# Kernel optimization log

Hardware: AMD Instinct MI355X
Metric: run time of the kernel (lower is better)

Reference implementation:

```python
import jax, jax.numpy as jnp
import numpy as np

B, S, D = 2, 2048, 768
HD = 64          # hardcoded head_dim in module
NH = D // HD     # 12 query heads
NKV = max(1, NH // 3)  # 4 kv heads
GROUPS = NH // NKV     # 3
WINDOW = 384
THETA = 10000.0
EPS = 1e-6


def setup_inputs() -> dict:
    key = jax.random.key(0)
    ks = jax.random.split(key, 5)
    return {
        "hidden_states": jax.random.normal(ks[0], (B, S, D), dtype=jnp.float32),
        "q_w": jax.random.normal(ks[1], (NH * HD, D), dtype=jnp.float32) * 0.02,
        "k_w": jax.random.normal(ks[2], (NKV * HD, D), dtype=jnp.float32) * 0.02,
        "v_w": jax.random.normal(ks[3], (NKV * HD, D), dtype=jnp.float32) * 0.02,
        "o_w": jax.random.normal(ks[4], (D, NH * HD), dtype=jnp.float32) * 0.02,
        "q_ln_w": jnp.ones((HD,), dtype=jnp.float32),
        "k_ln_w": jnp.ones((HD,), dtype=jnp.float32),
    }


def _rmsnorm(x, w):
    var = jnp.mean(jnp.square(x.astype(jnp.float32)), axis=-1, keepdims=True)
    return w * (x * jax.lax.rsqrt(var + EPS)).astype(x.dtype)


def _rotate_half(x):
    x1, x2 = jnp.split(x, 2, axis=-1)
    return jnp.concatenate((-x2, x1), axis=-1)


def _rope_cos_sin(seq_len, dtype):
    inv_freq = 1.0 / (THETA ** (jnp.arange(0, HD, 2, dtype=jnp.float32) / HD))
    t = jnp.arange(seq_len, dtype=jnp.float32)
    freqs = jnp.outer(t, inv_freq)            # [S, HD/2]
    emb = jnp.concatenate((freqs, freqs), -1)  # [S, HD]
    return jnp.cos(emb).astype(dtype), jnp.sin(emb).astype(dtype)


def reference(hidden_states, q_w, k_w, v_w, o_w, q_ln_w, k_ln_w):
    b, s, _ = hidden_states.shape
    # projections (nn.Linear: y = x @ W.T)
    q = hidden_states @ q_w.T   # [B,S,NH*HD]
    k = hidden_states @ k_w.T   # [B,S,NKV*HD]
    v = hidden_states @ v_w.T

    q = _rmsnorm(q.reshape(b, s, NH, HD), q_ln_w).transpose(0, 2, 1, 3)      # [B,NH,S,HD]
    k = _rmsnorm(k.reshape(b, s, NKV, HD), k_ln_w).transpose(0, 2, 1, 3)     # [B,NKV,S,HD]
    v = v.reshape(b, s, NKV, HD).transpose(0, 2, 1, 3)                       # [B,NKV,S,HD]

    cos, sin = _rope_cos_sin(s, q.dtype)  # [S,HD]
    cos = cos[None, None]
    sin = sin[None, None]
    q = q * cos + _rotate_half(q) * sin
    k = k * cos + _rotate_half(k) * sin

    # grouped-query repeat: [B,NKV,S,HD] -> [B,NH,S,HD]
    k = jnp.repeat(k, GROUPS, axis=1)
    v = jnp.repeat(v, GROUPS, axis=1)

    scores = jnp.einsum("bhqd,bhkd->bhqk", q, k) / np.sqrt(HD)
    # causal + sliding-window mask: allow i-WINDOW < j <= i
    idx = jnp.arange(s)
    rel = idx[None, :] - idx[:, None]  # j - i
    allowed = (rel <= 0) & (rel > -WINDOW)
    scores = jnp.where(allowed[None, None], scores, -jnp.inf)

    attn = jax.nn.softmax(scores.astype(jnp.float32), axis=-1).astype(q.dtype)
    out = jnp.einsum("bhqk,bhkd->bhqd", attn, v)       # [B,NH,S,HD]
    out = out.transpose(0, 2, 1, 3).reshape(b, s, NH * HD)
    return out @ o_w.T
```

## Files before the change

kernel.cpp:

```cpp
#include <hip/hip_runtime.h>
#include <hip/hip_bf16.h>

typedef __hip_bfloat16 bf16;
typedef __attribute__((ext_vector_type(8))) short bf16x8;
typedef __attribute__((ext_vector_type(4))) float f32x4;

#define MFMA16(a, b, c) __builtin_amdgcn_mfma_f32_16x16x32_bf16((a), (b), (c), 0, 0, 0)


__device__ __forceinline__ void st4bf(bf16* p, float4 v) {
    bf16 t[4];
    t[0] = __float2bfloat16(v.x); t[1] = __float2bfloat16(v.y);
    t[2] = __float2bfloat16(v.z); t[3] = __float2bfloat16(v.w);
    *reinterpret_cast<uint2*>(p) = *reinterpret_cast<const uint2*>(t);
}

__global__ __launch_bounds__(256) void k_prep(
    const float* __restrict__ hs, const float* __restrict__ qw,
    const float* __restrict__ kw, const float* __restrict__ vw,
    const float* __restrict__ ow,
    bf16* __restrict__ hsb, bf16* __restrict__ qwb, bf16* __restrict__ kwb,
    bf16* __restrict__ vwb, bf16* __restrict__ owb, float2* __restrict__ tab)
{
    const int bid = blockIdx.x, tid = threadIdx.x;
    const float* src; bf16* dst; int rel;
    if (bid < 3072)      { src = hs; dst = hsb; rel = bid; }
    else if (bid < 3648) { src = qw; dst = qwb; rel = bid - 3072; }
    else if (bid < 3840) { src = kw; dst = kwb; rel = bid - 3648; }
    else if (bid < 4032) { src = vw; dst = vwb; rel = bid - 3840; }
    else if (bid < 4608) { src = ow; dst = owb; rel = bid - 4032; }
    else {
        int i = (bid - 4608) * 256 + tid;
        int f = i & 31;
        float ang = (float)(i >> 5) * expf(-(float)f * 0.28782313662425572f);
        float sn, cs; sincosf(ang, &sn, &cs);
        tab[i] = make_float2(cs, sn);
        return;
    }
    int i = (rel * 256 + tid) * 4;
    float4 v = *reinterpret_cast<const float4*>(src + i);
    st4bf(dst + i, v);
}

__global__ __launch_bounds__(256) void k_qkv(
    const bf16* __restrict__ hsb, const bf16* __restrict__ qwb,
    const bf16* __restrict__ kwb, const bf16* __restrict__ vwb,
    const float* __restrict__ qln, const float* __restrict__ kln,
    const float2* __restrict__ tab,
    bf16* __restrict__ qo, bf16* __restrict__ ko, bf16* __restrict__ vto)
{
    __shared__ bf16 As[2][128 * 72];
    __shared__ bf16 Bs[2][128 * 72];
    const int tid = threadIdx.x;
    const int w = tid >> 6, l = tid & 63;
    const int lm = l & 15, lg = l >> 4;
    const int wr = w >> 1, wc = w & 1;
    const int m0 = blockIdx.x * 128;
    const int nblk = blockIdx.y;

    const bf16* wsrc; int kind, head;
    if (nblk < 6)      { wsrc = qwb + (size_t)nblk * 128 * 768;       kind = 0; head = nblk * 2 + wc; }
    else if (nblk < 8) { wsrc = kwb + (size_t)(nblk - 6) * 128 * 768; kind = 1; head = (nblk - 6) * 2 + wc; }
    else               { wsrc = vwb + (size_t)(nblk - 8) * 128 * 768; kind = 2; head = (nblk - 8) * 2 + wc; }

    const int sr = tid >> 1, scb = (tid & 1) * 8;
    const bf16* aptr = hsb  + (size_t)(m0 + sr) * 768 + scb;
    const bf16* bptr = wsrc + (size_t)sr * 768 + scb;

    bf16x8 ra[4], rb[4];
    #pragma unroll
    for (int j = 0; j < 4; ++j) {
        ra[j] = *(const bf16x8*)(aptr + j * 16);
        rb[j] = *(const bf16x8*)(bptr + j * 16);
    }
    #pragma unroll
    for (int j = 0; j < 4; ++j) {
        *(bf16x8*)(&As[0][sr * 72 + scb + j * 16]) = ra[j];
        *(bf16x8*)(&Bs[0][sr * 72 + scb + j * 16]) = rb[j];
    }
    __syncthreads();

    f32x4 acc[4][4] = {};
    for (int t = 0; t < 12; ++t) {
        const int p = t & 1;
        if (t < 11) {
            const int off = (t + 1) * 64;
            #pragma unroll
            for (int j = 0; j < 4; ++j) {
                ra[j] = *(const bf16x8*)(aptr + off + j * 16);
                rb[j] = *(const bf16x8*)(bptr + off + j * 16);
            }
        }
        #pragma unroll
        for (int kk = 0; kk < 2; ++kk) {
            bf16x8 af[4], bfv[4];
            #pragma unroll
            for (int mf = 0; mf < 4; ++mf)
                af[mf] = *(const bf16x8*)(&As[p][(wr * 64 + mf * 16 + lm) * 72 + kk * 32 + lg * 8]);
            #pragma unroll
            for (int ct = 0; ct < 4; ++ct)
                bfv[ct] = *(const bf16x8*)(&Bs[p][(wc * 64 + ct * 16 + lm) * 72 + kk * 32 + lg * 8]);
            #pragma unroll
            for (int mf = 0; mf < 4; ++mf)
                #pragma unroll
                for (int ct = 0; ct < 4; ++ct)
                    acc[mf][ct] = MFMA16(af[mf], bfv[ct], acc[mf][ct]);
        }
        if (t < 11) {
            __syncthreads();
            #pragma unroll
            for (int j = 0; j < 4; ++j) {
                *(bf16x8*)(&As[p ^ 1][sr * 72 + scb + j * 16]) = ra[j];
                *(bf16x8*)(&Bs[p ^ 1][sr * 72 + scb + j * 16]) = rb[j];
            }
            __syncthreads();
        }
    }

    const int b  = m0 >> 11;
    const int s0 = m0 & 2047;

    if (kind == 2) {
        bf16* base = vto + (size_t)(b * 4 + head) * 64 * 2048;
        #pragma unroll
        for (int mf = 0; mf < 4; ++mf)
            #pragma unroll
            for (int r = 0; r < 4; ++r) {
                const int s = s0 + wr * 64 + mf * 16 + lg * 4 + r;
                #pragma unroll
                for (int ct = 0; ct < 4; ++ct)
                    base[(size_t)(ct * 16 + lm) * 2048 + s] = __float2bfloat16(acc[mf][ct][r]);
            }
        return;
    }

    const float* ln = (kind == 0) ? qln : kln;
    float lw[4];
    #pragma unroll
    for (int ct = 0; ct < 4; ++ct) lw[ct] = ln[ct * 16 + lm];

    bf16* base = (kind == 0) ? qo + ((size_t)(b * 12 + head) * 2048 + s0) * 64
                             : ko + ((size_t)(b * 4  + head) * 2048 + s0) * 64;
    #pragma unroll
    for (int mf = 0; mf < 4; ++mf)
        #pragma unroll
        for (int r = 0; r < 4; ++r) {
            float n0 = acc[mf][0][r], n1 = acc[mf][1][r], n2 = acc[mf][2][r], n3 = acc[mf][3][r];
            float ss = n0 * n0 + n1 * n1 + n2 * n2 + n3 * n3;
            ss += __shfl_xor(ss, 1);
            ss += __shfl_xor(ss, 2);
            ss += __shfl_xor(ss, 4);
            ss += __shfl_xor(ss, 8);
            float rms = rsqrtf(ss * (1.0f / 64.0f) + 1e-6f);
            n0 *= rms * lw[0]; n1 *= rms * lw[1]; n2 *= rms * lw[2]; n3 *= rms * lw[3];
            const int row = wr * 64 + mf * 16 + lg * 4 + r;
            const float2* tp = tab + (size_t)(s0 + row) * 32;
            float2 t0 = tp[lm], t1 = tp[lm + 16];
            bf16* dst = base + (size_t)row * 64;
            dst[lm]      = __float2bfloat16(n0 * t0.x - n2 * t0.y);
            dst[lm + 16] = __float2bfloat16(n1 * t1.x - n3 * t1.y);
            dst[lm + 32] = __float2bfloat16(n2 * t0.x + n0 * t0.y);
            dst[lm + 48] = __float2bfloat16(n3 * t1.x + n1 * t1.y);
        }
}

__global__ __launch_bounds__(256) void k_attn(
    const bf16* __restrict__ qi, const bf16* __restrict__ ki,
    const bf16* __restrict__ vti, bf16* __restrict__ ao)
{
    __shared__ bf16 Ks[2][64 * 72];
    __shared__ bf16 Vs[2][64 * 72];
    __shared__ bf16 Ps[64 * 72];
    const int tid = threadIdx.x;
    const int w = tid >> 6, l = tid & 63;
    const int lm = l & 15, lg = l >> 4;
    const int qb = blockIdx.x, h = blockIdx.y, b = blockIdx.z;
    const int kv = h / 3;
    const int q0 = qb * 64;
    const float SCL2 = 0.18033688011117042f;

    const bf16* qbase = qi + ((size_t)((b * 12 + h) * 2048 + q0 + w * 16 + lm)) * 64 + lg * 8;
    bf16x8 qf0 = *(const bf16x8*)(qbase);
    bf16x8 qf1 = *(const bf16x8*)(qbase + 32);

    f32x4 oacc[4] = {};
    float m_[4], l_[4];
    #pragma unroll
    for (int r = 0; r < 4; ++r) { m_[r] = -INFINITY; l_[r] = 0.f; }

    const int sr = tid >> 2, sc = (tid & 3) * 16;
    const bf16* kgb = ki  + (size_t)(b * 4 + kv) * 2048 * 64;
    const bf16* vgb = vti + (size_t)(b * 4 + kv) * 64 * 2048;

    const int kb_lo = (qb > 6) ? (qb - 6) : 0;
    {
        const bf16* kp = kgb + (size_t)(kb_lo * 64 + sr) * 64 + sc;
        const bf16* vp = vgb + (size_t)sr * 2048 + kb_lo * 64 + sc;
        *(bf16x8*)(&Ks[0][sr * 72 + sc])     = *(const bf16x8*)(kp);
        *(bf16x8*)(&Ks[0][sr * 72 + sc + 8]) = *(const bf16x8*)(kp + 8);
        *(bf16x8*)(&Vs[0][sr * 72 + sc])     = *(const bf16x8*)(vp);
        *(bf16x8*)(&Vs[0][sr * 72 + sc + 8]) = *(const bf16x8*)(vp + 8);
    }
    __syncthreads();

    for (int kb = kb_lo; kb <= qb; ++kb) {
        const int p = (kb - kb_lo) & 1;
        const int k0 = kb * 64;

        bf16x8 rk0, rk1, rv0, rv1;
        if (kb < qb) {
            const bf16* kp = kgb + (size_t)(k0 + 64 + sr) * 64 + sc;
            const bf16* vp = vgb + (size_t)sr * 2048 + k0 + 64 + sc;
            rk0 = *(const bf16x8*)(kp);
            rk1 = *(const bf16x8*)(kp + 8);
            rv0 = *(const bf16x8*)(vp);
            rv1 = *(const bf16x8*)(vp + 8);
        }

        f32x4 sacc[4];
        #pragma unroll
        for (int kt = 0; kt < 4; ++kt) {
            bf16x8 kf0 = *(const bf16x8*)(&Ks[p][(kt * 16 + lm) * 72 + lg * 8]);
            bf16x8 kf1 = *(const bf16x8*)(&Ks[p][(kt * 16 + lm) * 72 + 32 + lg * 8]);
            f32x4 z = {0.f, 0.f, 0.f, 0.f};
            z = MFMA16(qf0, kf0, z);
            sacc[kt] = MFMA16(qf1, kf1, z);
        }

        float pmax[4] = {-INFINITY, -INFINITY, -INFINITY, -INFINITY};
        #pragma unroll
        for (int kt = 0; kt < 4; ++kt)
            #pragma unroll
            for (int r = 0; r < 4; ++r) {
                int kgl = k0 + kt * 16 + lm;
                int qgl = q0 + w * 16 + lg * 4 + r;
                bool ok = (kgl <= qgl) && (kgl > qgl - 384);
                float s = ok ? sacc[kt][r] * SCL2 : -INFINITY;
                sacc[kt][r] = s;
                pmax[r] = fmaxf(pmax[r], s);
            }
        #pragma unroll
        for (int r = 0; r < 4; ++r) {
            float t = pmax[r];
            t = fmaxf(t, __shfl_xor(t, 1));
            t = fmaxf(t, __shfl_xor(t, 2));
            t = fmaxf(t, __shfl_xor(t, 4));
            t = fmaxf(t, __shfl_xor(t, 8));
            pmax[r] = t;
        }

        #pragma unroll
        for (int r = 0; r < 4; ++r) {
            float mnew = fmaxf(m_[r], pmax[r]);
            float scale, rs = 0.f, pv[4];
            if (mnew > -INFINITY) {
                scale = exp2f(m_[r] - mnew);
                #pragma unroll
                for (int kt = 0; kt < 4; ++kt) { pv[kt] = exp2f(sacc[kt][r] - mnew); rs += pv[kt]; }
            } else {
                scale = 1.f;
                #pragma unroll
                for (int kt = 0; kt < 4; ++kt) pv[kt] = 0.f;
            }
            m_[r] = mnew;
            rs += __shfl_xor(rs, 1);
            rs += __shfl_xor(rs, 2);
            rs += __shfl_xor(rs, 4);
            rs += __shfl_xor(rs, 8);
            l_[r] = l_[r] * scale + rs;
            #pragma unroll
            for (int dt = 0; dt < 4; ++dt) oacc[dt][r] *= scale;
            #pragma unroll
            for (int kt = 0; kt < 4; ++kt)
                Ps[(w * 16 + lg * 4 + r) * 72 + kt * 16 + lm] = __float2bfloat16(pv[kt]);
        }

        bf16x8 pf0 = *(const bf16x8*)(&Ps[(w * 16 + lm) * 72 + lg * 8]);
        bf16x8 pf1 = *(const bf16x8*)(&Ps[(w * 16 + lm) * 72 + 32 + lg * 8]);
        #pragma unroll
        for (int dt = 0; dt < 4; ++dt) {
            bf16x8 vf0 = *(const bf16x8*)(&Vs[p][(dt * 16 + lm) * 72 + lg * 8]);
            bf16x8 vf1 = *(const bf16x8*)(&Vs[p][(dt * 16 + lm) * 72 + 32 + lg * 8]);
            oacc[dt] = MFMA16(pf0, vf0, oacc[dt]);
            oacc[dt] = MFMA16(pf1, vf1, oacc[dt]);
        }

        if (kb < qb) {
            __syncthreads();
            *(bf16x8*)(&Ks[p ^ 1][sr * 72 + sc])     = rk0;
            *(bf16x8*)(&Ks[p ^ 1][sr * 72 + sc + 8]) = rk1;
            *(bf16x8*)(&Vs[p ^ 1][sr * 72 + sc])     = rv0;
            *(bf16x8*)(&Vs[p ^ 1][sr * 72 + sc + 8]) = rv1;
            __syncthreads();
        }
    }

    #pragma unroll
    for (int r = 0; r < 4; ++r) {
        float inv = 1.f / l_[r];
        bf16* dst = ao + ((size_t)(b * 2048 + q0 + w * 16 + lg * 4 + r)) * 768 + h * 64;
        #pragma unroll
        for (int dt = 0; dt < 4; ++dt)
            dst[dt * 16 + lm] = __float2bfloat16(oacc[dt][r] * inv);
    }
}

__global__ __launch_bounds__(256) void k_oproj(
    const bf16* __restrict__ A, const bf16* __restrict__ W, float* __restrict__ out)
{
    __shared__ bf16 As[2][128 * 72];
    __shared__ bf16 Bs[2][128 * 72];
    const int tid = threadIdx.x;
    const int w = tid >> 6, l = tid & 63;
    const int lm = l & 15, lg = l >> 4;
    const int wr = w >> 1, wc = w & 1;
    const int m0 = blockIdx.x * 128, n0 = blockIdx.y * 128;

    const int sr = tid >> 1, scb = (tid & 1) * 8;
    const bf16* aptr = A + (size_t)(m0 + sr) * 768 + scb;
    const bf16* bptr = W + (size_t)(n0 + sr) * 768 + scb;

    bf16x8 ra[4], rb[4];
    #pragma unroll
    for (int j = 0; j < 4; ++j) {
        ra[j] = *(const bf16x8*)(aptr + j * 16);
        rb[j] = *(const bf16x8*)(bptr + j * 16);
    }
    #pragma unroll
    for (int j = 0; j < 4; ++j) {
        *(bf16x8*)(&As[0][sr * 72 + scb + j * 16]) = ra[j];
        *(bf16x8*)(&Bs[0][sr * 72 + scb + j * 16]) = rb[j];
    }
    __syncthreads();

    f32x4 acc[4][4] = {};
    for (int t = 0; t < 12; ++t) {
        const int p = t & 1;
        if (t < 11) {
            const int off = (t + 1) * 64;
            #pragma unroll
            for (int j = 0; j < 4; ++j) {
                ra[j] = *(const bf16x8*)(aptr + off + j * 16);
                rb[j] = *(const bf16x8*)(bptr + off + j * 16);
            }
        }
        #pragma unroll
        for (int kk = 0; kk < 2; ++kk) {
            bf16x8 af[4], bfv[4];
            #pragma unroll
            for (int mf = 0; mf < 4; ++mf)
                af[mf] = *(const bf16x8*)(&As[p][(wr * 64 + mf * 16 + lm) * 72 + kk * 32 + lg * 8]);
            #pragma unroll
            for (int ct = 0; ct < 4; ++ct)
                bfv[ct] = *(const bf16x8*)(&Bs[p][(wc * 64 + ct * 16 + lm) * 72 + kk * 32 + lg * 8]);
            #pragma unroll
            for (int mf = 0; mf < 4; ++mf)
                #pragma unroll
                for (int ct = 0; ct < 4; ++ct)
                    acc[mf][ct] = MFMA16(af[mf], bfv[ct], acc[mf][ct]);
        }
        if (t < 11) {
            __syncthreads();
            #pragma unroll
            for (int j = 0; j < 4; ++j) {
                *(bf16x8*)(&As[p ^ 1][sr * 72 + scb + j * 16]) = ra[j];
                *(bf16x8*)(&Bs[p ^ 1][sr * 72 + scb + j * 16]) = rb[j];
            }
            __syncthreads();
        }
    }

    #pragma unroll
    for (int mf = 0; mf < 4; ++mf)
        #pragma unroll
        for (int r = 0; r < 4; ++r) {
            float* dst = out + (size_t)(m0 + wr * 64 + mf * 16 + lg * 4 + r) * 768 + n0 + wc * 64;
            #pragma unroll
            for (int ct = 0; ct < 4; ++ct)
                dst[ct * 16 + lm] = acc[mf][ct][r];
        }
}

extern "C" void kernel_launch(void* const* d_in, const int* in_sizes, int n_in,
                              void* d_out, int out_size, void* d_ws, size_t ws_size,
                              hipStream_t stream) {
    const float* hs  = (const float*)d_in[0];
    const float* qw  = (const float*)d_in[1];
    const float* kw  = (const float*)d_in[2];
    const float* vw  = (const float*)d_in[3];
    const float* ow  = (const float*)d_in[4];
    const float* qln = (const float*)d_in[5];
    const float* kln = (const float*)d_in[6];
    float* out = (float*)d_out;

    float2* tab  = (float2*)d_ws;
    bf16*   q_ws = (bf16*)(tab + 65536);
    bf16*   k_ws = q_ws + 3145728;
    bf16*   vt_ws= k_ws + 1048576;
    bf16*   x_ws = vt_ws + 1048576;
    bf16*   qwb  = x_ws + 3145728;
    bf16*   kwb  = qwb + 589824;
    bf16*   vwb  = kwb + 196608;
    bf16*   owb  = vwb + 196608;

    k_prep<<<dim3(4864), 256, 0, stream>>>(hs, qw, kw, vw, ow, x_ws, qwb, kwb, vwb, owb, tab);
    k_qkv<<<dim3(32, 10, 1), 256, 0, stream>>>(x_ws, qwb, kwb, vwb, qln, kln, tab, q_ws, k_ws, vt_ws);
    k_attn<<<dim3(32, 12, 2), 256, 0, stream>>>(q_ws, k_ws, vt_ws, x_ws);
    k_oproj<<<dim3(32, 6, 1), 256, 0, stream>>>(x_ws, owb, out);
}
```

Measured before the change: 74.70 us.

## Load attention K/V and o-proj operands directly from global memory, dropping LDS staging

In the attention kernel, the double-buffered shared-memory K/V tiles and their barriers are removed. Each wave now reads its MFMA K and V fragments straight from global memory. The o-projection GEMM does the same for its A and W tiles. This removes LDS traffic and __syncthreads, but it loses cross-wave reuse and explicit prefetching, so performance depends on L1/L2 caching and exposed global-load latency.

```diff
diff --git a/kernel.cpp b/kernel.cpp
--- a/kernel.cpp
+++ b/kernel.cpp
@@ -168,8 +168,6 @@
     const bf16* __restrict__ qi, const bf16* __restrict__ ki,
     const bf16* __restrict__ vti, bf16* __restrict__ ao)
 {
-    __shared__ bf16 Ks[2][64 * 72];
-    __shared__ bf16 Vs[2][64 * 72];
     __shared__ bf16 Ps[64 * 72];
     const int tid = threadIdx.x;
     const int w = tid >> 6, l = tid & 63;
@@ -188,40 +186,19 @@
     #pragma unroll
     for (int r = 0; r < 4; ++r) { m_[r] = -INFINITY; l_[r] = 0.f; }
 
-    const int sr = tid >> 2, sc = (tid & 3) * 16;
-    const bf16* kgb = ki  + (size_t)(b * 4 + kv) * 2048 * 64;
-    const bf16* vgb = vti + (size_t)(b * 4 + kv) * 64 * 2048;
+    const bf16* krow = ki  + (size_t)(b * 4 + kv) * 2048 * 64 + (size_t)lm * 64 + lg * 8;
+    const bf16* vrow = vti + (size_t)(b * 4 + kv) * 64 * 2048 + (size_t)lm * 2048 + lg * 8;
 
     const int kb_lo = (qb > 6) ? (qb - 6) : 0;
-    {
-        const bf16* kp = kgb + (size_t)(kb_lo * 64 + sr) * 64 + sc;
-        const bf16* vp = vgb + (size_t)sr * 2048 + kb_lo * 64 + sc;
-        *(bf16x8*)(&Ks[0][sr * 72 + sc])     = *(const bf16x8*)(kp);
-        *(bf16x8*)(&Ks[0][sr * 72 + sc + 8]) = *(const bf16x8*)(kp + 8);
-        *(bf16x8*)(&Vs[0][sr * 72 + sc])     = *(const bf16x8*)(vp);
-        *(bf16x8*)(&Vs[0][sr * 72 + sc + 8]) = *(const bf16x8*)(vp + 8);
-    }
-    __syncthreads();
-
     for (int kb = kb_lo; kb <= qb; ++kb) {
-        const int p = (kb - kb_lo) & 1;
         const int k0 = kb * 64;
 
-        bf16x8 rk0, rk1, rv0, rv1;
-        if (kb < qb) {
-            const bf16* kp = kgb + (size_t)(k0 + 64 + sr) * 64 + sc;
-            const bf16* vp = vgb + (size_t)sr * 2048 + k0 + 64 + sc;
-            rk0 = *(const bf16x8*)(kp);
-            rk1 = *(const bf16x8*)(kp + 8);
-            rv0 = *(const bf16x8*)(vp);
-            rv1 = *(const bf16x8*)(vp + 8);
-        }
-
         f32x4 sacc[4];
         #pragma unroll
         for (int kt = 0; kt < 4; ++kt) {
-            bf16x8 kf0 = *(const bf16x8*)(&Ks[p][(kt * 16 + lm) * 72 + lg * 8]);
-            bf16x8 kf1 = *(const bf16x8*)(&Ks[p][(kt * 16 + lm) * 72 + 32 + lg * 8]);
+            const bf16* kp = krow + (size_t)(k0 + kt * 16) * 64;
+            bf16x8 kf0 = *(const bf16x8*)(kp);
+            bf16x8 kf1 = *(const bf16x8*)(kp + 32);
             f32x4 z = {0.f, 0.f, 0.f, 0.f};
             z = MFMA16(qf0, kf0, z);
             sacc[kt] = MFMA16(qf1, kf1, z);
@@ -279,19 +256,11 @@
         bf16x8 pf1 = *(const bf16x8*)(&Ps[(w * 16 + lm) * 72 + 32 + lg * 8]);
         #pragma unroll
         for (int dt = 0; dt < 4; ++dt) {
-            bf16x8 vf0 = *(const bf16x8*)(&Vs[p][(dt * 16 + lm) * 72 + lg * 8]);
-            bf16x8 vf1 = *(const bf16x8*)(&Vs[p][(dt * 16 + lm) * 72 + 32 + lg * 8]);
+            const bf16* vp = vrow + (size_t)(dt * 16) * 2048 + k0;
+            bf16x8 vf0 = *(const bf16x8*)(vp);
+            bf16x8 vf1 = *(const bf16x8*)(vp + 32);
             oacc[dt] = MFMA16(pf0, vf0, oacc[dt]);
             oacc[dt] = MFMA16(pf1, vf1, oacc[dt]);
-        }
-
-        if (kb < qb) {
-            __syncthreads();
-            *(bf16x8*)(&Ks[p ^ 1][sr * 72 + sc])     = rk0;
-            *(bf16x8*)(&Ks[p ^ 1][sr * 72 + sc + 8]) = rk1;
-            *(bf16x8*)(&Vs[p ^ 1][sr * 72 + sc])     = rv0;
-            *(bf16x8*)(&Vs[p ^ 1][sr * 72 + sc + 8]) = rv1;
-            __syncthreads();
         }
     }
 
@@ -308,65 +277,35 @@
 __global__ __launch_bounds__(256) void k_oproj(
     const bf16* __restrict__ A, const bf16* __restrict__ W, float* __restrict__ out)
 {
-    __shared__ bf16 As[2][128 * 72];
-    __shared__ bf16 Bs[2][128 * 72];
     const int tid = threadIdx.x;
     const int w = tid >> 6, l = tid & 63;
     const int lm = l & 15, lg = l >> 4;
     const int wr = w >> 1, wc = w & 1;
     const int m0 = blockIdx.x * 128, n0 = blockIdx.y * 128;
 
-    const int sr = tid >> 1, scb = (tid & 1) * 8;
-    const bf16* aptr = A + (size_t)(m0 + sr) * 768 + scb;
-    const bf16* bptr = W + (size_t)(n0 + sr) * 768 + scb;
-
-    bf16x8 ra[4], rb[4];
-    #pragma unroll
-    for (int j = 0; j < 4; ++j) {
-        ra[j] = *(const bf16x8*)(aptr + j * 16);
-        rb[j] = *(const bf16x8*)(bptr + j * 16);
-    }
-    #pragma unroll
-    for (int j = 0; j < 4; ++j) {
-        *(bf16x8*)(&As[0][sr * 72 + scb + j * 16]) = ra[j];
-        *(bf16x8*)(&Bs[0][sr * 72 + scb + j * 16]) = rb[j];
-    }
-    __syncthreads();
+    const bf16* arow[4];
+    const bf16* brow[4];
+    #pragma unroll
+    for (int i = 0; i < 4; ++i) {
+        arow[i] = A + (size_t)(m0 + wr * 64 + i * 16 + lm) * 768 + lg * 8;
+        brow[i] = W + (size_t)(n0 + wc * 64 + i * 16 + lm) * 768 + lg * 8;
+    }
 
     f32x4 acc[4][4] = {};
     for (int t = 0; t < 12; ++t) {
-        const int p = t & 1;
-        if (t < 11) {
-            const int off = (t + 1) * 64;
-            #pragma unroll
-            for (int j = 0; j < 4; ++j) {
-                ra[j] = *(const bf16x8*)(aptr + off + j * 16);
-                rb[j] = *(const bf16x8*)(bptr + off + j * 16);
-            }
-        }
         #pragma unroll
         for (int kk = 0; kk < 2; ++kk) {
+            const int off = t * 64 + kk * 32;
             bf16x8 af[4], bfv[4];
             #pragma unroll
-            for (int mf = 0; mf < 4; ++mf)
-                af[mf] = *(const bf16x8*)(&As[p][(wr * 64 + mf * 16 + lm) * 72 + kk * 32 + lg * 8]);
-            #pragma unroll
-            for (int ct = 0; ct < 4; ++ct)
-                bfv[ct] = *(const bf16x8*)(&Bs[p][(wc * 64 + ct * 16 + lm) * 72 + kk * 32 + lg * 8]);
+            for (int mf = 0; mf < 4; ++mf) af[mf]  = *(const bf16x8*)(arow[mf] + off);
+            #pragma unroll
+            for (int ct = 0; ct < 4; ++ct) bfv[ct] = *(const bf16x8*)(brow[ct] + off);
             #pragma unroll
             for (int mf = 0; mf < 4; ++mf)
                 #pragma unroll
                 for (int ct = 0; ct < 4; ++ct)
                     acc[mf][ct] = MFMA16(af[mf], bfv[ct], acc[mf][ct]);
-        }
-        if (t < 11) {
-            __syncthreads();
-            #pragma unroll
-            for (int j = 0; j < 4; ++j) {
-                *(bf16x8*)(&As[p ^ 1][sr * 72 + scb + j * 16]) = ra[j];
-                *(bf16x8*)(&Bs[p ^ 1][sr * 72 + scb + j * 16]) = rb[j];
-            }
-            __syncthreads();
         }
     }
 
```

Measured after the change: 101.8 us. +36.2%, slower.
